# Performance work log

Hardware: AMD Instinct MI355X
Metric: run time of the kernel (lower is better)

Reference implementation:

```python
import jax, jax.numpy as jnp
import numpy as np

NUM_HEADS = 8
NUM_KV_HEADS = 1
HEAD_DIM = 256
ROPE_THETA = 10000.0


def setup_inputs() -> dict:
    key = jax.random.key(0)
    ks = jax.random.split(key, 5)
    B, S, H = 4, 2048, 2048
    hidden_states = jax.random.normal(ks[0], (B, S, H), dtype=jnp.float32)
    # Linear weights stored as (in_features, out_features); y = x @ W
    scale = 0.02
    Wq = jax.random.normal(ks[1], (H, NUM_HEADS * HEAD_DIM), dtype=jnp.float32) * scale
    Wk = jax.random.normal(ks[2], (H, NUM_KV_HEADS * HEAD_DIM), dtype=jnp.float32) * scale
    Wv = jax.random.normal(ks[3], (H, NUM_KV_HEADS * HEAD_DIM), dtype=jnp.float32) * scale
    Wo = jax.random.normal(ks[4], (NUM_HEADS * HEAD_DIM, H), dtype=jnp.float32) * scale
    position_ids = jnp.broadcast_to(jnp.arange(S, dtype=jnp.int64), (B, S))
    return {"hidden_states": hidden_states, "Wq": Wq, "Wk": Wk, "Wv": Wv,
            "Wo": Wo, "position_ids": position_ids}


def _rotate_half(x):
    h = x.shape[-1] // 2
    return jnp.concatenate([-x[..., h:], x[..., :h]], axis=-1)


def _rope_cos_sin(position_ids, head_dim, theta):
    # inv_freq: [head_dim/2]
    inv_freq = 1.0 / (theta ** (jnp.arange(0, head_dim, 2, dtype=jnp.float32) / head_dim))
    freqs = position_ids.astype(jnp.float32)[..., None] * inv_freq  # [B,S,hd/2]
    emb = jnp.concatenate([freqs, freqs], axis=-1)                   # [B,S,hd]
    # shape [B,1,S,hd] to broadcast over heads
    return jnp.cos(emb)[:, None], jnp.sin(emb)[:, None]


def reference(hidden_states, Wq, Wk, Wv, Wo, position_ids):
    B, S, H = hidden_states.shape
    groups = NUM_HEADS // NUM_KV_HEADS

    q = (hidden_states @ Wq).reshape(B, S, NUM_HEADS, HEAD_DIM).transpose(0, 2, 1, 3)
    k = (hidden_states @ Wk).reshape(B, S, NUM_KV_HEADS, HEAD_DIM).transpose(0, 2, 1, 3)
    v = (hidden_states @ Wv).reshape(B, S, NUM_KV_HEADS, HEAD_DIM).transpose(0, 2, 1, 3)

    cos, sin = _rope_cos_sin(position_ids, HEAD_DIM, ROPE_THETA)
    q = q * cos + _rotate_half(q) * sin
    k = k * cos + _rotate_half(k) * sin

    # GQA: repeat kv heads to match query heads
    k = jnp.repeat(k, groups, axis=1)  # [B,Hq,S,hd]
    v = jnp.repeat(v, groups, axis=1)

    scores = jnp.einsum('bhqd,bhkd->bhqk', q, k) / jnp.sqrt(jnp.float32(HEAD_DIM))
    causal = position_ids[:, None, :, None] >= position_ids[:, None, None, :]  # [B,1,S,S]
    scores = jnp.where(causal, scores, jnp.float32(-1e9))
    attn = jax.nn.softmax(scores, axis=-1)

    out = jnp.einsum('bhqk,bhkd->bhqd', attn, v)             # [B,H,S,hd]
    out = out.transpose(0, 2, 1, 3).reshape(B, S, NUM_HEADS * HEAD_DIM)
    return out @ Wo
```

## Files before the change

kernel.cpp:

```cpp
#include <hip/hip_runtime.h>
#include <hip/hip_bf16.h>

typedef __bf16 bf16;
typedef __bf16 bf16x8 __attribute__((ext_vector_type(8)));
typedef __bf16 bf16x4 __attribute__((ext_vector_type(4)));
typedef float f32x4 __attribute__((ext_vector_type(4)));

#define NB 4
#define SEQ 2048
#define HID 2048
#define NHEAD 8
#define HDIM 256
#define MTOT (NB*SEQ)

#define WAIT_VM8()  asm volatile("s_waitcnt vmcnt(8)" ::: "memory")
#define WAIT_VM5()  asm volatile("s_waitcnt vmcnt(5)" ::: "memory")
#define WAIT_VM0()  asm volatile("s_waitcnt vmcnt(0)" ::: "memory")

__device__ __forceinline__ void gl_lds16(const void* g, void* l) {
  __builtin_amdgcn_global_load_lds(
      (const __attribute__((address_space(1))) void*)g,
      (__attribute__((address_space(3))) void*)l, 16, 0, 0);
}

__global__ __launch_bounds__(256)
void prologue_kernel(const float* __restrict__ hs, bf16* __restrict__ Xb,
                     const float* __restrict__ Wq, bf16* __restrict__ WqT,
                     const float* __restrict__ Wo, bf16* __restrict__ WoT,
                     const float* __restrict__ Wk, bf16* __restrict__ WkT,
                     const float* __restrict__ Wv, bf16* __restrict__ WvT,
                     float2* __restrict__ tab)
{
  __shared__ float tile[32][33];
  const int bid = blockIdx.x;
  const int t = threadIdx.x;

  if (bid < 8192) {
    size_t i = (size_t)(bid * 256 + t) * 8;
    float4 v0 = *(const float4*)(hs + i);
    float4 v1 = *(const float4*)(hs + i + 4);
    bf16x8 o;
    o[0]=(bf16)v0.x; o[1]=(bf16)v0.y; o[2]=(bf16)v0.z; o[3]=(bf16)v0.w;
    o[4]=(bf16)v1.x; o[5]=(bf16)v1.y; o[6]=(bf16)v1.z; o[7]=(bf16)v1.w;
    *(bf16x8*)(Xb + i) = o;
  } else if (bid < 17408) {
    const float* in; bf16* out; int R, C, bx, by;
    if (bid < 16384) {
      int id = bid - 8192;
      int z = id >> 12, r = id & 4095;
      in = z ? Wo : Wq; out = z ? WoT : WqT; R = 2048; C = 2048;
      bx = (r & 63) * 32; by = (r >> 6) * 32;
    } else {
      int id = bid - 16384;
      int z = id >> 9, r = id & 511;
      in = z ? Wv : Wk; out = z ? WvT : WkT; R = 2048; C = 256;
      bx = (r & 7) * 32; by = (r >> 3) * 32;
    }
    int tx = t & 31, ty = t >> 5;
    #pragma unroll
    for (int k = 0; k < 4; k++)
      tile[ty + 8*k][tx] = in[(size_t)(by + ty + 8*k) * C + bx + tx];
    __syncthreads();
    #pragma unroll
    for (int k = 0; k < 4; k++)
      out[(size_t)(bx + ty + 8*k) * R + by + tx] = (bf16)tile[tx][ty + 8*k];
  } else {
    int i = (bid - 17408) * 256 + t;
    int s = i >> 7, p = i & 127;
    float invf = powf(10000.0f, -(float)p * (1.0f / 128.0f));
    float ang = (float)s * invf;
    float sn, cs;
    sincosf(ang, &sn, &cs);
    tab[i] = make_float2(cs, sn);
  }
}

template<int EPI>
__global__ __launch_bounds__(512, 2)
void gemm256_kernel(const bf16* __restrict__ A, const bf16* __restrict__ Bt,
                    void* __restrict__ Cout, int N, int K,
                    const float2* __restrict__ tab,
                    const bf16* __restrict__ Bt2,
                    bf16* __restrict__ Kout, bf16* __restrict__ VTout)
{
  __shared__ bf16 Albs[2][256 * 64];
  __shared__ bf16 Blbs[2][256 * 64];
  const int t = threadIdx.x, lane = t & 63, w = t >> 6;
  const int g = lane >> 4, c = lane & 15;
  const int wm = w >> 2, wn = w & 3;

  const int L = blockIdx.x + 8 * blockIdx.y;
  const int xcd = L & 7, slot = L >> 3;
  const int m0 = (xcd * 4 + (slot >> 3)) * 256;
  const int n0 = (slot & 7) * 256;

  const bf16* Ab = A + (size_t)m0 * K;
  const bf16* Bb = Bt + (size_t)n0 * K;

  auto stage = [&](const bf16* G, int k0, bf16* lds) {
    #pragma unroll
    for (int it = 0; it < 4; ++it) {
      int slot2 = it * 512 + t;
      int row = slot2 >> 3, part = (slot2 & 7) ^ (row & 7);
      gl_lds16(G + (size_t)row * K + k0 + part * 8, lds + (it * 512 + w * 64) * 8);
    }
  };

  f32x4 acc[8][4];
  #pragma unroll
  for (int i = 0; i < 8; i++)
    #pragma unroll
    for (int j = 0; j < 4; j++)
      acc[i][j] = (f32x4){0.f, 0.f, 0.f, 0.f};

  stage(Ab, 0, &Albs[0][0]);
  stage(Bb, 0, &Blbs[0][0]);
  __builtin_amdgcn_sched_barrier(0);

  const int NT = K >> 6;
  #pragma unroll 1
  for (int kt = 0; kt < NT; ++kt) {
    const int buf = kt & 1;
    if (kt + 1 < NT) {
      stage(Ab, (kt + 1) * 64, &Albs[buf ^ 1][0]);
      stage(Bb, (kt + 1) * 64, &Blbs[buf ^ 1][0]);
    }
    __builtin_amdgcn_sched_barrier(0);
    if (kt + 1 < NT) { WAIT_VM8(); } else { WAIT_VM0(); }
    __builtin_amdgcn_s_barrier();
    __builtin_amdgcn_sched_barrier(0);

    #pragma unroll
    for (int s2 = 0; s2 < 2; s2++) {
      bf16x8 bfr[4];
      #pragma unroll
      for (int j = 0; j < 4; j++) {
        int row = (EPI == 4) ? (wn * 16 + (j & 1) * 64 + (j >> 1) * 128 + c)
                             : (wn * 64 + j * 16 + c);
        bfr[j] = *(const bf16x8*)((const char*)&Blbs[buf][0] + row * 128 +
                                  ((s2 * 64 + g * 16) ^ ((c & 7) * 16)));
      }
      #pragma unroll
      for (int i = 0; i < 8; i++) {
        int row = wm * 128 + i * 16 + c;
        const bf16x8 af = *(const bf16x8*)((const char*)&Albs[buf][0] + row * 128 +
                                           ((s2 * 64 + g * 16) ^ ((c & 7) * 16)));
        #pragma unroll
        for (int j = 0; j < 4; j++)
          acc[i][j] = __builtin_amdgcn_mfma_f32_16x16x32_bf16(af, bfr[j], acc[i][j], 0, 0, 0);
      }
    }
    __builtin_amdgcn_s_barrier();
  }

  if constexpr (EPI == 4) {
    #pragma unroll
    for (int i = 0; i < 8; i++) {
      #pragma unroll
      for (int rr = 0; rr < 4; rr++) {
        int m = m0 + wm * 128 + i * 16 + g * 4 + rr;
        int s = m & (SEQ - 1);
        bf16* orow = (bf16*)Cout + (size_t)m * N + n0;
        #pragma unroll
        for (int jp = 0; jp < 2; jp++) {
          int d = wn * 16 + jp * 64 + c;
          float2 cs = tab[s * 128 + d];
          float vlo = acc[i][jp][rr], vhi = acc[i][jp | 2][rr];
          orow[d]       = (bf16)(vlo * cs.x - vhi * cs.y);
          orow[d + 128] = (bf16)(vhi * cs.x + vlo * cs.y);
        }
      }
    }

    WAIT_VM0();
    __builtin_amdgcn_s_barrier();
    __builtin_amdgcn_sched_barrier(0);

    const int kvm0 = xcd * 1024 + (slot >> 1) * 64;
    const int kvc = slot & 1;
    const bf16* A2 = A + (size_t)kvm0 * K;
    const bf16* B2 = Bt2 + (size_t)(kvc * 256) * K;

    auto stageA2 = [&](int k0, bf16* lds) {
      int row = t >> 3, part = (t & 7) ^ (row & 7);
      gl_lds16(A2 + (size_t)row * K + k0 + part * 8, lds + (w * 64) * 8);
    };

    f32x4 acc2[2][4];
    #pragma unroll
    for (int i = 0; i < 2; i++)
      #pragma unroll
      for (int j = 0; j < 4; j++)
        acc2[i][j] = (f32x4){0.f, 0.f, 0.f, 0.f};

    stageA2(0, &Albs[0][0]);
    stage(B2, 0, &Blbs[0][0]);
    __builtin_amdgcn_sched_barrier(0);

    #pragma unroll 1
    for (int kt = 0; kt < NT; ++kt) {
      const int buf = kt & 1;
      if (kt + 1 < NT) {
        stageA2((kt + 1) * 64, &Albs[buf ^ 1][0]);
        stage(B2, (kt + 1) * 64, &Blbs[buf ^ 1][0]);
      }
      __builtin_amdgcn_sched_barrier(0);
      if (kt + 1 < NT) { WAIT_VM5(); } else { WAIT_VM0(); }
      __builtin_amdgcn_s_barrier();
      __builtin_amdgcn_sched_barrier(0);

      #pragma unroll
      for (int s2 = 0; s2 < 2; s2++) {
        bf16x8 bfr[4];
        #pragma unroll
        for (int j = 0; j < 4; j++) {
          int row = wn * 16 + (j & 1) * 64 + (j >> 1) * 128 + c;
          bfr[j] = *(const bf16x8*)((const char*)&Blbs[buf][0] + row * 128 +
                                    ((s2 * 64 + g * 16) ^ ((c & 7) * 16)));
        }
        #pragma unroll
        for (int i = 0; i < 2; i++) {
          int row = wm * 32 + i * 16 + c;
          const bf16x8 af = *(const bf16x8*)((const char*)&Albs[buf][0] + row * 128 +
                                             ((s2 * 64 + g * 16) ^ ((c & 7) * 16)));
          #pragma unroll
          for (int j = 0; j < 4; j++)
            acc2[i][j] = __builtin_amdgcn_mfma_f32_16x16x32_bf16(af, bfr[j], acc2[i][j], 0, 0, 0);
        }
      }
      __builtin_amdgcn_s_barrier();
    }

    if (kvc == 0) {
      #pragma unroll
      for (int i = 0; i < 2; i++) {
        #pragma unroll
        for (int rr = 0; rr < 4; rr++) {
          int m = kvm0 + wm * 32 + i * 16 + g * 4 + rr;
          int s = m & (SEQ - 1);
          bf16* orow = Kout + (size_t)m * 256;
          #pragma unroll
          for (int jp = 0; jp < 2; jp++) {
            int d = wn * 16 + jp * 64 + c;
            float2 cs = tab[s * 128 + d];
            float vlo = acc2[i][jp][rr], vhi = acc2[i][jp | 2][rr];
            orow[d]       = (bf16)(vlo * cs.x - vhi * cs.y);
            orow[d + 128] = (bf16)(vhi * cs.x + vlo * cs.y);
          }
        }
      }
    } else {
      #pragma unroll
      for (int i = 0; i < 2; i++) {
        #pragma unroll
        for (int rr = 0; rr < 4; rr++) {
          int m = kvm0 + wm * 32 + i * 16 + g * 4 + rr;
          int b = m >> 11, s = m & 2047;
          #pragma unroll
          for (int j = 0; j < 4; j++) {
            int cl = wn * 16 + (j & 1) * 64 + (j >> 1) * 128 + c;
            VTout[((size_t)b * 256 + cl) * SEQ + s] = (bf16)acc2[i][j][rr];
          }
        }
      }
    }
  } else {
    #pragma unroll
    for (int i = 0; i < 8; i++) {
      #pragma unroll
      for (int j = 0; j < 4; j++) {
        #pragma unroll
        for (int rr = 0; rr < 4; rr++) {
          int m = m0 + wm * 128 + i * 16 + g * 4 + rr;
          int col = n0 + wn * 64 + j * 16 + c;
          float v = acc[i][j][rr];
          if constexpr (EPI == 0) ((bf16*)Cout)[(size_t)m * N + col] = (bf16)v;
          else                    ((float*)Cout)[(size_t)m * N + col] = v;
        }
      }
    }
  }
}

__global__ __launch_bounds__(512, 2)
void attn_kernel(const bf16* __restrict__ Q, const bf16* __restrict__ Kb,
                 const bf16* __restrict__ VT, bf16* __restrict__ O)
{
  __shared__ bf16 Klds[2][64 * 256];
  __shared__ bf16 Vlds[2][256 * 64];
  __shared__ bf16 Plds[8][16 * 64];

  const int L = blockIdx.x + ((int)gridDim.x) * blockIdx.y;
  const int xcd = L & 7, slot = L >> 3;
  const int b = xcd >> 1;
  const int rem = ((xcd & 1) << 5) | slot;
  const int h = rem >> 3;
  const int p = rem & 7;

  const int t = threadIdx.x, lane = t & 63, w = t >> 6;
  const int g = lane >> 4, c = lane & 15;

  const bf16* Kbase = Kb + (size_t)b * SEQ * HDIM;
  const bf16* Vbase = VT + (size_t)b * HDIM * SEQ;

  bf16x8 ones8;
  #pragma unroll
  for (int z = 0; z < 8; z++) ones8[z] = (bf16)1.0f;

  auto stageK = [&](int kt, int buf) {
    const int kv0 = kt * 64;
    #pragma unroll
    for (int it = 0; it < 4; ++it) {
      int slot2 = it * 512 + t;
      int krow = slot2 >> 5, kpart = (slot2 & 31) ^ (krow & 7);
      gl_lds16(Kbase + (size_t)(kv0 + krow) * HDIM + kpart * 8,
               &Klds[buf][0] + (it * 512 + w * 64) * 8);
    }
  };
  auto stageV = [&](int kt, int buf) {
    const int kv0 = kt * 64;
    #pragma unroll
    for (int it = 0; it < 4; ++it) {
      int slot2 = it * 512 + t;
      int vrow = slot2 >> 3, vpart = (slot2 & 7) ^ (vrow & 7);
      gl_lds16(Vbase + (size_t)vrow * SEQ + kv0 + vpart * 8,
               &Vlds[buf][0] + (it * 512 + w * 64) * 8);
    }
  };

  #pragma unroll 1
  for (int pass = 0; pass < 2; ++pass) {
    const int qt = pass ? (15 - p) : p;
    const int q0 = qt * 128;
    const int last = 2 * qt + 1;

    bf16x8 qf[8];
    const bf16* qp = Q + (size_t)(b * SEQ + q0 + w * 16 + c) * (NHEAD * HDIM) + h * HDIM + g * 8;
    #pragma unroll
    for (int s = 0; s < 8; s++) qf[s] = *(const bf16x8*)(qp + s * 32);
    __builtin_amdgcn_sched_barrier(0);

    stageK(0, 0);
    stageV(0, 0);
    __builtin_amdgcn_sched_barrier(0);

    f32x4 acc[16];
    #pragma unroll
    for (int f = 0; f < 16; f++) acc[f] = (f32x4){0.f, 0.f, 0.f, 0.f};
    f32x4 acc_s = (f32x4){0.f, 0.f, 0.f, 0.f};

    #pragma unroll 1
    for (int kt = 0; kt <= last; ++kt) {
      const int kv0 = kt * 64;
      const int buf = kt & 1;

      if (kt < last) { stageK(kt + 1, buf ^ 1); stageV(kt + 1, buf ^ 1); }
      __builtin_amdgcn_sched_barrier(0);
      if (kt < last) { WAIT_VM8(); } else { WAIT_VM0(); }
      __builtin_amdgcn_s_barrier();
      __builtin_amdgcn_sched_barrier(0);

      const int qrow_min = q0 + w * 16;
      if (kv0 <= qrow_min + 15) {
        f32x4 sc[4];
        #pragma unroll
        for (int j = 0; j < 4; j++) sc[j] = (f32x4){0.f, 0.f, 0.f, 0.f};
        __builtin_amdgcn_s_setprio(1);
        #pragma unroll
        for (int s = 0; s < 8; s++) {
          #pragma unroll
          for (int j = 0; j < 4; j++) {
            const bf16x8 kf = *(const bf16x8*)((const char*)&Klds[buf][0] + (j * 16 + c) * 512 +
                                               ((s * 64 + g * 16) ^ ((c & 7) * 16)));
            sc[j] = __builtin_amdgcn_mfma_f32_16x16x32_bf16(qf[s], kf, sc[j], 0, 0, 0);
          }
        }
        __builtin_amdgcn_s_setprio(0);

        const float C1 = 0.09016844f;
        const float C2 = 11.54156036f;
        const bool diag = (kv0 + 63 > qrow_min);
        #pragma unroll
        for (int rr = 0; rr < 4; rr++) {
          const int row = g * 4 + rr;
          const int qrow = qrow_min + row;
          #pragma unroll
          for (int j = 0; j < 4; j++) {
            float e = exp2f(__builtin_fmaf(sc[j][rr], C1, -C2));
            if (diag && (kv0 + j * 16 + c > qrow)) e = 0.f;
            *(bf16*)((char*)&Plds[w][0] + row * 128 + (((j * 32) + c * 2) ^ ((row & 7) << 4))) = (bf16)e;
          }
        }

        #pragma unroll
        for (int s2 = 0; s2 < 2; s2++) {
          const bf16x8 pf = *(const bf16x8*)((const char*)&Plds[w][0] + c * 128 +
                                             (((s2 * 4 + g) << 4) ^ ((c & 7) << 4)));
          __builtin_amdgcn_s_setprio(1);
          #pragma unroll
          for (int f = 0; f < 16; f++) {
            const bf16x8 vf = *(const bf16x8*)((const char*)&Vlds[buf][0] + (f * 16 + c) * 128 +
                                               ((s2 * 64 + g * 16) ^ ((c & 7) * 16)));
            acc[f] = __builtin_amdgcn_mfma_f32_16x16x32_bf16(pf, vf, acc[f], 0, 0, 0);
          }
          acc_s = __builtin_amdgcn_mfma_f32_16x16x32_bf16(pf, ones8, acc_s, 0, 0, 0);
          __builtin_amdgcn_s_setprio(0);
        }
      }

      __builtin_amdgcn_s_barrier();
    }

    #pragma unroll
    for (int rr = 0; rr < 4; rr++) {
      float inv = 1.0f / acc_s[rr];
      #pragma unroll
      for (int f = 0; f < 16; f++) {
        float v = acc[f][rr] * inv;
        O[(size_t)(b * SEQ + q0 + w * 16 + g * 4 + rr) * (NHEAD * HDIM) + h * HDIM + f * 16 + c] = (bf16)v;
      }
    }
  }
}

extern "C" void kernel_launch(void* const* d_in, const int* in_sizes, int n_in,
                              void* d_out, int out_size, void* d_ws, size_t ws_size,
                              hipStream_t stream) {
  const float* hs = (const float*)d_in[0];
  const float* Wq = (const float*)d_in[1];
  const float* Wk = (const float*)d_in[2];
  const float* Wv = (const float*)d_in[3];
  const float* Wo = (const float*)d_in[4];

  char* ws = (char*)d_ws;
  bf16* Xb   = (bf16*)(ws + 0);
  bf16* WqT  = (bf16*)(ws + 33554432);
  bf16* WkT  = (bf16*)(ws + 41943040);
  bf16* WvT  = (bf16*)(ws + 42991616);
  bf16* WoT  = (bf16*)(ws + 44040192);
  bf16* Qb   = (bf16*)(ws + 52428800);
  bf16* Kb   = (bf16*)(ws + 85983232);
  bf16* VTb  = (bf16*)(ws + 90177536);
  float2* tab = (float2*)(ws + 94371840);

  prologue_kernel<<<18432, 256, 0, stream>>>(hs, Xb, Wq, WqT, Wo, WoT,
                                             Wk, WkT, Wv, WvT, tab);

  gemm256_kernel<4><<<dim3(8, 32), 512, 0, stream>>>(Xb, WqT, (void*)Qb, 2048, 2048,
                                                     tab, WkT, Kb, VTb);

  attn_kernel<<<dim3(8, 32), 512, 0, stream>>>(Qb, Kb, VTb, Xb );

  gemm256_kernel<2><<<dim3(8, 32), 512, 0, stream>>>(Xb, WoT, d_out, 2048, 2048,
                                                     nullptr, nullptr, nullptr, nullptr);
}
```

Baseline: 299.9 us.

## Interleave next-tile global loads with MFMA phases in GEMM main loop

```diff
diff --git a/kernel.cpp b/kernel.cpp
--- a/kernel.cpp
+++ b/kernel.cpp
@@ -15,7 +15,9 @@
 
 #define WAIT_VM8()  asm volatile("s_waitcnt vmcnt(8)" ::: "memory")
 #define WAIT_VM5()  asm volatile("s_waitcnt vmcnt(5)" ::: "memory")
+#define WAIT_VM2()  asm volatile("s_waitcnt vmcnt(2)" ::: "memory")
 #define WAIT_VM0()  asm volatile("s_waitcnt vmcnt(0)" ::: "memory")
+#define LGKM0()     asm volatile("s_waitcnt lgkmcnt(0)" ::: "memory")
 
 __device__ __forceinline__ void gl_lds16(const void* g, void* l) {
   __builtin_amdgcn_global_load_lds(
@@ -97,13 +99,21 @@
   const bf16* Ab = A + (size_t)m0 * K;
   const bf16* Bb = Bt + (size_t)n0 * K;
 
-  auto stage = [&](const bf16* G, int k0, bf16* lds) {
-    #pragma unroll
-    for (int it = 0; it < 4; ++it) {
-      int slot2 = it * 512 + t;
-      int row = slot2 >> 3, part = (slot2 & 7) ^ (row & 7);
-      gl_lds16(G + (size_t)row * K + k0 + part * 8, lds + (it * 512 + w * 64) * 8);
-    }
+  auto stage_q = [&](const bf16* G, int k0, bf16* lds, int it) {
+    int slot2 = it * 512 + t;
+    int row = slot2 >> 3, part = (slot2 & 7) ^ (row & 7);
+    gl_lds16(G + (size_t)row * K + k0 + part * 8, lds + (it * 512 + w * 64) * 8);
+  };
+  auto readA = [&](int buf, int i, int ks) -> bf16x8 {
+    int row = wm * 128 + i * 16 + c;
+    return *(const bf16x8*)((const char*)&Albs[buf][0] + row * 128 +
+                            ((ks * 64 + g * 16) ^ ((c & 7) * 16)));
+  };
+  auto readB = [&](int buf, int j, int ks) -> bf16x8 {
+    int row = (EPI == 4) ? (wn * 16 + (j & 1) * 64 + (j >> 1) * 128 + c)
+                         : (wn * 64 + j * 16 + c);
+    return *(const bf16x8*)((const char*)&Blbs[buf][0] + row * 128 +
+                            ((ks * 64 + g * 16) ^ ((c & 7) * 16)));
   };
 
   f32x4 acc[8][4];
@@ -113,44 +123,94 @@
     for (int j = 0; j < 4; j++)
       acc[i][j] = (f32x4){0.f, 0.f, 0.f, 0.f};
 
-  stage(Ab, 0, &Albs[0][0]);
-  stage(Bb, 0, &Blbs[0][0]);
+  #pragma unroll
+  for (int q = 0; q < 4; q++) {
+    stage_q(Ab, 0, &Albs[0][0], q);
+    stage_q(Bb, 0, &Blbs[0][0], q);
+  }
   __builtin_amdgcn_sched_barrier(0);
 
   const int NT = K >> 6;
   #pragma unroll 1
-  for (int kt = 0; kt < NT; ++kt) {
-    const int buf = kt & 1;
-    if (kt + 1 < NT) {
-      stage(Ab, (kt + 1) * 64, &Albs[buf ^ 1][0]);
-      stage(Bb, (kt + 1) * 64, &Blbs[buf ^ 1][0]);
-    }
-    __builtin_amdgcn_sched_barrier(0);
-    if (kt + 1 < NT) { WAIT_VM8(); } else { WAIT_VM0(); }
-    __builtin_amdgcn_s_barrier();
-    __builtin_amdgcn_sched_barrier(0);
-
-    #pragma unroll
-    for (int s2 = 0; s2 < 2; s2++) {
-      bf16x8 bfr[4];
-      #pragma unroll
-      for (int j = 0; j < 4; j++) {
-        int row = (EPI == 4) ? (wn * 16 + (j & 1) * 64 + (j >> 1) * 128 + c)
-                             : (wn * 64 + j * 16 + c);
-        bfr[j] = *(const bf16x8*)((const char*)&Blbs[buf][0] + row * 128 +
-                                  ((s2 * 64 + g * 16) ^ ((c & 7) * 16)));
-      }
-      #pragma unroll
-      for (int i = 0; i < 8; i++) {
-        int row = wm * 128 + i * 16 + c;
-        const bf16x8 af = *(const bf16x8*)((const char*)&Albs[buf][0] + row * 128 +
-                                           ((s2 * 64 + g * 16) ^ ((c & 7) * 16)));
-        #pragma unroll
-        for (int j = 0; j < 4; j++)
-          acc[i][j] = __builtin_amdgcn_mfma_f32_16x16x32_bf16(af, bfr[j], acc[i][j], 0, 0, 0);
-      }
-    }
-    __builtin_amdgcn_s_barrier();
+  for (int T = 0; T < NT; ++T) {
+    const int buf = T & 1;
+    const bool more = (T + 1 < NT);
+    const int kn = (T + 1) * 64;
+    bf16x8 af[4], bk[4];
+
+    if (more) { stage_q(Ab, kn, &Albs[buf ^ 1][0], 0); stage_q(Bb, kn, &Blbs[buf ^ 1][0], 0); }
+    __builtin_amdgcn_sched_barrier(0);
+    if (more) { WAIT_VM2(); } else { WAIT_VM0(); }
+    __builtin_amdgcn_s_barrier();
+    __builtin_amdgcn_sched_barrier(0);
+    #pragma unroll
+    for (int i = 0; i < 4; i++) af[i] = readA(buf, i, 0);
+    #pragma unroll
+    for (int j = 0; j < 4; j++) bk[j] = readB(buf, j, 0);
+    LGKM0();
+    __builtin_amdgcn_sched_barrier(0);
+    __builtin_amdgcn_s_setprio(1);
+    #pragma unroll
+    for (int i = 0; i < 4; i++)
+      #pragma unroll
+      for (int j = 0; j < 4; j++)
+        acc[i][j] = __builtin_amdgcn_mfma_f32_16x16x32_bf16(af[i], bk[j], acc[i][j], 0, 0, 0);
+    __builtin_amdgcn_s_setprio(0);
+    __builtin_amdgcn_s_barrier();
+    __builtin_amdgcn_sched_barrier(0);
+
+    #pragma unroll
+    for (int i = 0; i < 4; i++) af[i] = readA(buf, 4 + i, 0);
+    if (more) { stage_q(Ab, kn, &Albs[buf ^ 1][0], 1); stage_q(Bb, kn, &Blbs[buf ^ 1][0], 1); }
+    __builtin_amdgcn_sched_barrier(0);
+    __builtin_amdgcn_s_barrier();
+    LGKM0();
+    __builtin_amdgcn_sched_barrier(0);
+    __builtin_amdgcn_s_setprio(1);
+    #pragma unroll
+    for (int i = 0; i < 4; i++)
+      #pragma unroll
+      for (int j = 0; j < 4; j++)
+        acc[4 + i][j] = __builtin_amdgcn_mfma_f32_16x16x32_bf16(af[i], bk[j], acc[4 + i][j], 0, 0, 0);
+    __builtin_amdgcn_s_setprio(0);
+    __builtin_amdgcn_s_barrier();
+    __builtin_amdgcn_sched_barrier(0);
+
+    #pragma unroll
+    for (int i = 0; i < 4; i++) af[i] = readA(buf, i, 1);
+    #pragma unroll
+    for (int j = 0; j < 4; j++) bk[j] = readB(buf, j, 1);
+    if (more) { stage_q(Ab, kn, &Albs[buf ^ 1][0], 2); stage_q(Bb, kn, &Blbs[buf ^ 1][0], 2); }
+    __builtin_amdgcn_sched_barrier(0);
+    __builtin_amdgcn_s_barrier();
+    LGKM0();
+    __builtin_amdgcn_sched_barrier(0);
+    __builtin_amdgcn_s_setprio(1);
+    #pragma unroll
+    for (int i = 0; i < 4; i++)
+      #pragma unroll
+      for (int j = 0; j < 4; j++)
+        acc[i][j] = __builtin_amdgcn_mfma_f32_16x16x32_bf16(af[i], bk[j], acc[i][j], 0, 0, 0);
+    __builtin_amdgcn_s_setprio(0);
+    __builtin_amdgcn_s_barrier();
+    __builtin_amdgcn_sched_barrier(0);
+
+    #pragma unroll
+    for (int i = 0; i < 4; i++) af[i] = readA(buf, 4 + i, 1);
+    if (more) { stage_q(Ab, kn, &Albs[buf ^ 1][0], 3); stage_q(Bb, kn, &Blbs[buf ^ 1][0], 3); }
+    __builtin_amdgcn_sched_barrier(0);
+    __builtin_amdgcn_s_barrier();
+    LGKM0();
+    __builtin_amdgcn_sched_barrier(0);
+    __builtin_amdgcn_s_setprio(1);
+    #pragma unroll
+    for (int i = 0; i < 4; i++)
+      #pragma unroll
+      for (int j = 0; j < 4; j++)
+        acc[4 + i][j] = __builtin_amdgcn_mfma_f32_16x16x32_bf16(af[i], bk[j], acc[4 + i][j], 0, 0, 0);
+    __builtin_amdgcn_s_setprio(0);
+    __builtin_amdgcn_s_barrier();
+    __builtin_amdgcn_sched_barrier(0);
   }
 
   if constexpr (EPI == 4) {
@@ -185,6 +245,10 @@
       int row = t >> 3, part = (t & 7) ^ (row & 7);
       gl_lds16(A2 + (size_t)row * K + k0 + part * 8, lds + (w * 64) * 8);
     };
+    auto stageB2 = [&](int k0, bf16* lds) {
+      #pragma unroll
+      for (int q = 0; q < 4; q++) stage_q(B2, k0, lds, q);
+    };
 
     f32x4 acc2[2][4];
     #pragma unroll
@@ -194,7 +258,7 @@
         acc2[i][j] = (f32x4){0.f, 0.f, 0.f, 0.f};
 
     stageA2(0, &Albs[0][0]);
-    stage(B2, 0, &Blbs[0][0]);
+    stageB2(0, &Blbs[0][0]);
     __builtin_amdgcn_sched_barrier(0);
 
     #pragma unroll 1
@@ -202,7 +266,7 @@
       const int buf = kt & 1;
       if (kt + 1 < NT) {
         stageA2((kt + 1) * 64, &Albs[buf ^ 1][0]);
-        stage(B2, (kt + 1) * 64, &Blbs[buf ^ 1][0]);
+        stageB2((kt + 1) * 64, &Blbs[buf ^ 1][0]);
       }
       __builtin_amdgcn_sched_barrier(0);
       if (kt + 1 < NT) { WAIT_VM5(); } else { WAIT_VM0(); }
@@ -221,11 +285,11 @@
         #pragma unroll
         for (int i = 0; i < 2; i++) {
           int row = wm * 32 + i * 16 + c;
-          const bf16x8 af = *(const bf16x8*)((const char*)&Albs[buf][0] + row * 128 +
-                                             ((s2 * 64 + g * 16) ^ ((c & 7) * 16)));
+          const bf16x8 af2 = *(const bf16x8*)((const char*)&Albs[buf][0] + row * 128 +
+                                              ((s2 * 64 + g * 16) ^ ((c & 7) * 16)));
           #pragma unroll
           for (int j = 0; j < 4; j++)
-            acc2[i][j] = __builtin_amdgcn_mfma_f32_16x16x32_bf16(af, bfr[j], acc2[i][j], 0, 0, 0);
+            acc2[i][j] = __builtin_amdgcn_mfma_f32_16x16x32_bf16(af2, bfr[j], acc2[i][j], 0, 0, 0);
         }
       }
       __builtin_amdgcn_s_barrier();
```

Measured after the change: 308.8 us. 3.0% more time.
